# Kernel tuning notes

Hardware: AMD Instinct MI355X
Metric: run time of the kernel (lower is better)

The kernel has to match this reference:

```python
import jax, jax.numpy as jnp
import numpy as np

B, H, S, D = 8, 16, 1024, 128


def setup_inputs() -> dict:
    key = jax.random.key(0)
    kq, kk, kv = jax.random.split(key, 3)
    queries = jax.random.normal(kq, (B, H, S, D), dtype=jnp.float32)
    keys = jax.random.normal(kk, (B, H, S, D), dtype=jnp.float32)
    values = jax.random.normal(kv, (B, H, S, D), dtype=jnp.float32)
    # learnable per-element scale over the full score tensor, init 'ones'
    scale = jnp.ones((B, H, S, S), dtype=jnp.float32)
    return {"queries": queries, "keys": keys, "values": values, "scale": scale}


def reference(queries, keys, values, scale):
    # scores: [B,H,Sq,Sk] = Q K^T
    scores = jnp.einsum("bhqd,bhkd->bhqk", queries, keys)
    # custom learnable scaling: scores / sqrt(scale[0]) * scale
    # scale[0] has shape [H,Sq,Sk] and broadcasts over the batch dim
    scores = scores / jnp.sqrt(scale[0]) * scale
    # masked_softmax with attention_mask=None -> plain softmax over keys axis
    attn = jax.nn.softmax(scores, axis=-1)
    # dropout is identity (rate 0 / eval mode)
    out = jnp.einsum("bhqk,bhkd->bhqd", attn, values)
    return out
```

## Files before the change

kernel.cpp:

```cpp
#include <hip/hip_runtime.h>
#include <math.h>

#define NB 8
#define NH 16
#define NS 1024
#define ND 128

typedef float    f32x4 __attribute__((ext_vector_type(4)));
typedef _Float16 f16x8 __attribute__((ext_vector_type(8)));
typedef _Float16 f16x4 __attribute__((ext_vector_type(4)));
typedef short    s16x4 __attribute__((ext_vector_type(4)));
typedef short    s16x8 __attribute__((ext_vector_type(8)));

#define MFMAH(a, b, c) __builtin_amdgcn_mfma_f32_16x16x32_f16(a, b, c, 0, 0, 0)

__device__ __forceinline__ void gload16(const void* g, void* l) {
  __builtin_amdgcn_global_load_lds(
      (const __attribute__((address_space(1))) void*)g,
      (__attribute__((address_space(3))) void*)l, 16, 0, 0);
}

__global__ void prep_e(const float* __restrict__ scale, _Float16* __restrict__ E) {
  const size_t i0 = ((size_t)blockIdx.x * 256 + threadIdx.x) * 8;
  float4 a0 = *(const float4*)(scale + i0);
  float4 b0 = *(const float4*)(scale + i0 + 4);
  float r[8] = {rsqrtf(a0.x), rsqrtf(a0.y), rsqrtf(a0.z), rsqrtf(a0.w),
                rsqrtf(b0.x), rsqrtf(b0.y), rsqrtf(b0.z), rsqrtf(b0.w)};
#pragma unroll
  for (int b = 0; b < NB; ++b) {
    const float* sp = scale + ((size_t)b << 24) + i0;
    float4 a = *(const float4*)sp;
    float4 bb = *(const float4*)(sp + 4);
    f16x8 o = {(_Float16)(a.x * r[0]), (_Float16)(a.y * r[1]),
               (_Float16)(a.z * r[2]), (_Float16)(a.w * r[3]),
               (_Float16)(bb.x * r[4]), (_Float16)(bb.y * r[5]),
               (_Float16)(bb.z * r[6]), (_Float16)(bb.w * r[7])};
    *(f16x8*)(E + ((size_t)b << 24) + i0) = o;
  }
}

__global__ void prep_k(const float* __restrict__ K, short* __restrict__ Kimg) {
  const int kt = blockIdx.x & 15, bh = blockIdx.x >> 4;
  const float* Kt = K + ((size_t)bh * NS + kt * 64) * ND;
  short* img = Kimg + ((size_t)bh * 16 + kt) * 8192;
#pragma unroll
  for (int i = 0; i < 8; ++i) {
    int f = threadIdx.x + i * 256;
    int key = f >> 5, d4 = (f & 31) << 2;
    float4 v = *(const float4*)(Kt + (size_t)key * ND + d4);
    f16x4 hv = {(_Float16)v.x, (_Float16)v.y, (_Float16)v.z, (_Float16)v.w};
    int gp = (d4 >> 3) ^ (key & 15);
    *(f16x4*)(img + key * 128 + gp * 8 + (d4 & 7)) = hv;
  }
}

__global__ void prep_v(const float* __restrict__ V, short* __restrict__ Vimg) {
  __shared__ _Float16 t[64 * 132];
  const int kt = blockIdx.x & 15, bh = blockIdx.x >> 4;
  const float* Vt = V + ((size_t)bh * NS + kt * 64) * ND;
#pragma unroll
  for (int i = 0; i < 8; ++i) {
    int f = threadIdx.x + i * 256;
    int key = f >> 5, d4 = (f & 31) << 2;
    float4 v = *(const float4*)(Vt + (size_t)key * ND + d4);
    *(f16x4*)&t[key * 132 + d4] =
        (f16x4){(_Float16)v.x, (_Float16)v.y, (_Float16)v.z, (_Float16)v.w};
  }
  __syncthreads();
  short* img = Vimg + ((size_t)bh * 16 + kt) * 8192;
#pragma unroll
  for (int i = 0; i < 4; ++i) {
    int u = threadIdx.x + i * 256;
    int d = u >> 3, g = u & 7;
    f16x8 o;
#pragma unroll
    for (int e = 0; e < 8; ++e) o[e] = t[(g * 8 + e) * 132 + d];
    *(f16x8*)(img + d * 64 + ((g ^ (d & 7)) * 8)) = o;
  }
}

template <bool USE_E>
__launch_bounds__(256, 3)
__global__ void attn_f16(const float* __restrict__ Q, const short* __restrict__ Kimg,
                         const short* __restrict__ Vimg, const _Float16* __restrict__ E,
                         const float* __restrict__ scale, float* __restrict__ out) {
  __shared__ short Ks[64 * 128];
  __shared__ short Vs[128 * 64];
  __shared__ _Float16 Ps[128 * 72];

  const int tid = threadIdx.x;
  const int w = tid >> 6, l = tid & 63;
  const int quad = l >> 4, c = l & 15;

  const int x = blockIdx.x;
  const int bh = ((x >> 6) << 3) | (x & 7);
  const int qblk = (x >> 3) & 7;
  const int q0 = qblk * 128 + w * 32;

  f16x8 qf[2][4];
  {
    const float* Qb = Q + ((size_t)bh * NS + q0) * ND;
#pragma unroll
    for (int nf = 0; nf < 2; ++nf)
#pragma unroll
      for (int kb = 0; kb < 4; ++kb) {
        const float* p = Qb + (size_t)(nf * 16 + c) * ND + kb * 32 + quad * 8;
        float4 a = *(const float4*)p;
        float4 b = *(const float4*)(p + 4);
        qf[nf][kb] = (f16x8){(_Float16)a.x, (_Float16)a.y, (_Float16)a.z, (_Float16)a.w,
                             (_Float16)b.x, (_Float16)b.y, (_Float16)b.z, (_Float16)b.w};
      }
  }

  float m_[2] = {-INFINITY, -INFINITY}, ls_[2] = {0.f, 0.f};
  f32x4 O[2][8];
#pragma unroll
  for (int pf = 0; pf < 2; ++pf)
#pragma unroll
    for (int n0 = 0; n0 < 8; ++n0) O[pf][n0] = (f32x4){0.f, 0.f, 0.f, 0.f};

  const short* Kb = Kimg + (size_t)bh * (16 * 8192);
  const short* Vb = Vimg + (size_t)bh * (16 * 8192);
  const _Float16* Eb = E + ((size_t)bh << 20);
  const float* sclb = scale + ((size_t)bh << 20);
  const float* sc0b = scale + ((size_t)(bh & 15) << 20);

#pragma unroll 1
  for (int kt = 0; kt < 16; ++kt) {
    __syncthreads();
    {
      const short* kg = Kb + kt * 8192 + tid * 8;
      const short* vg = Vb + kt * 8192 + tid * 8;
#pragma unroll
      for (int i = 0; i < 4; ++i) {
        gload16(kg + i * 2048, &Ks[tid * 8 + i * 2048]);
        gload16(vg + i * 2048, &Vs[tid * 8 + i * 2048]);
      }
    }
    f16x4 ef[2][4];
    f32x4 sclv[2][4], sc0v[2][4];
    if (USE_E) {
#pragma unroll
      for (int nf = 0; nf < 2; ++nf)
#pragma unroll
        for (int m0 = 0; m0 < 4; ++m0)
          ef[nf][m0] = *(const f16x4*)(Eb + (size_t)(q0 + nf * 16 + c) * NS +
                                       kt * 64 + m0 * 16 + quad * 4);
    } else {
#pragma unroll
      for (int nf = 0; nf < 2; ++nf)
#pragma unroll
        for (int m0 = 0; m0 < 4; ++m0) {
          size_t off = (size_t)(q0 + nf * 16 + c) * NS + kt * 64 + m0 * 16 + quad * 4;
          sclv[nf][m0] = *(const f32x4*)(sclb + off);
          sc0v[nf][m0] = *(const f32x4*)(sc0b + off);
        }
    }
    __syncthreads();

    f32x4 S[2][4];
#pragma unroll
    for (int nf = 0; nf < 2; ++nf)
#pragma unroll
      for (int m0 = 0; m0 < 4; ++m0) S[nf][m0] = (f32x4){0.f, 0.f, 0.f, 0.f};
#pragma unroll
    for (int m0 = 0; m0 < 4; ++m0) {
#pragma unroll
      for (int kb = 0; kb < 4; ++kb) {
        const f16x8 a = *(const f16x8*)&Ks[(m0 * 16 + c) * 128 + ((((kb << 2) | quad)) ^ c) * 8];
        S[0][m0] = MFMAH(a, qf[0][kb], S[0][m0]);
        S[1][m0] = MFMAH(a, qf[1][kb], S[1][m0]);
      }
    }

    float al2[2];
#pragma unroll
    for (int nf = 0; nf < 2; ++nf) {
      float sv[16];
#pragma unroll
      for (int m0 = 0; m0 < 4; ++m0)
#pragma unroll
        for (int r = 0; r < 4; ++r) {
          float e = USE_E ? (float)ef[nf][m0][r]
                          : sclv[nf][m0][r] * rsqrtf(sc0v[nf][m0][r]);
          sv[m0 * 4 + r] = S[nf][m0][r] * e;
        }
      float tm = sv[0];
#pragma unroll
      for (int i = 1; i < 16; ++i) tm = fmaxf(tm, sv[i]);
      tm = fmaxf(tm, __shfl_xor(tm, 16));
      tm = fmaxf(tm, __shfl_xor(tm, 32));
      float mn = fmaxf(m_[nf], tm);
      float al = __expf(m_[nf] - mn);
      float ps = 0.f;
      _Float16 pb[16];
#pragma unroll
      for (int i = 0; i < 16; ++i) {
        float p = __expf(sv[i] - mn);
        ps += p;
        pb[i] = (_Float16)p;
      }
      ps += __shfl_xor(ps, 16);
      ps += __shfl_xor(ps, 32);
      ls_[nf] = ls_[nf] * al + ps;
      m_[nf] = mn;
      al2[nf] = al;
      _Float16* pr = &Ps[(size_t)(w * 32 + nf * 16 + c) * 72];
#pragma unroll
      for (int m0 = 0; m0 < 4; ++m0)
        *(f16x4*)(pr + m0 * 16 + quad * 4) =
            (f16x4){pb[m0 * 4], pb[m0 * 4 + 1], pb[m0 * 4 + 2], pb[m0 * 4 + 3]};
    }

#pragma unroll
    for (int pf = 0; pf < 2; ++pf) {
      float ar[4];
#pragma unroll
      for (int r = 0; r < 4; ++r) ar[r] = __shfl(al2[pf], quad * 4 + r);
#pragma unroll
      for (int n0 = 0; n0 < 8; ++n0)
#pragma unroll
        for (int r = 0; r < 4; ++r) O[pf][n0][r] *= ar[r];
    }

    f16x8 pfr[2][2];
#pragma unroll
    for (int pf = 0; pf < 2; ++pf)
#pragma unroll
      for (int kb = 0; kb < 2; ++kb)
        pfr[pf][kb] = *(const f16x8*)&Ps[(size_t)(w * 32 + pf * 16 + c) * 72 +
                                         kb * 32 + quad * 8];
#pragma unroll
    for (int n0 = 0; n0 < 8; ++n0) {
#pragma unroll
      for (int kb = 0; kb < 2; ++kb) {
        const f16x8 b =
            *(const f16x8*)&Vs[(n0 * 16 + c) * 64 + ((((kb << 2) | quad)) ^ (c & 7)) * 8];
        O[0][n0] = MFMAH(pfr[0][kb], b, O[0][n0]);
        O[1][n0] = MFMAH(pfr[1][kb], b, O[1][n0]);
      }
    }
  }

  float* ob = out + ((size_t)bh * NS + q0) * ND;
#pragma unroll
  for (int pf = 0; pf < 2; ++pf)
#pragma unroll
    for (int r = 0; r < 4; ++r) {
      float lv = __shfl(ls_[pf], quad * 4 + r);
      float inv = 1.0f / lv;
      int row = pf * 16 + quad * 4 + r;
#pragma unroll
      for (int n0 = 0; n0 < 8; ++n0)
        ob[(size_t)row * ND + n0 * 16 + c] = O[pf][n0][r] * inv;
    }
}

#define TQ 16
#define TK 64
#define PITCH 129
__launch_bounds__(256, 2)
__global__ void attn_fp32(const float* __restrict__ Q, const float* __restrict__ K,
                          const float* __restrict__ V, const float* __restrict__ scale,
                          float* __restrict__ out) {
  __shared__ float qs[TQ][ND];
  __shared__ float kv[TK][PITCH];
  __shared__ float ps[4][4][TK];
  const int tid = threadIdx.x;
  const int w = tid >> 6, l = tid & 63;
  const int bid = blockIdx.x;
  const int qt = bid & 63, h = (bid >> 6) & 15, b = bid >> 10;
  const size_t bh = (size_t)b * NH + h;
  const float* Qb = Q + (bh * NS + (size_t)qt * TQ) * ND;
  const float* Kb = K + bh * NS * ND;
  const float* Vb = V + bh * NS * ND;
  {
    const float4* Q4 = (const float4*)Qb;
    float4* qs4 = (float4*)&qs[0][0];
    qs4[tid] = Q4[tid];
    qs4[tid + 256] = Q4[tid + 256];
  }
  const int q0 = qt * TQ + w * 4;
  const float* sc0p[4];
  const float* sclp[4];
#pragma unroll
  for (int i = 0; i < 4; ++i) {
    const int qg = q0 + i;
    sc0p[i] = scale + ((size_t)h * NS + qg) * NS;
    sclp[i] = scale + (bh * NS + qg) * NS;
  }
  float m[4] = {-INFINITY, -INFINITY, -INFINITY, -INFINITY};
  float lsum[4] = {0.f, 0.f, 0.f, 0.f};
  float oa[4] = {0.f, 0.f, 0.f, 0.f};
  float ob[4] = {0.f, 0.f, 0.f, 0.f};
  for (int kt = 0; kt < NS / TK; ++kt) {
    __syncthreads();
    {
      const float4* K4 = (const float4*)(Kb + (size_t)kt * TK * ND);
#pragma unroll
      for (int i = 0; i < 8; ++i) {
        const int f = tid + i * 256;
        const float4 t4 = K4[f];
        const int r = f >> 5, cc = (f & 31) << 2;
        kv[r][cc] = t4.x; kv[r][cc + 1] = t4.y; kv[r][cc + 2] = t4.z; kv[r][cc + 3] = t4.w;
      }
    }
    __syncthreads();
    const int kg = kt * TK + l;
    float sc0[4], scl[4];
#pragma unroll
    for (int i = 0; i < 4; ++i) { sc0[i] = sc0p[i][kg]; scl[i] = sclp[i][kg]; }
    float s[4] = {0.f, 0.f, 0.f, 0.f};
#pragma unroll 8
    for (int d = 0; d < ND; ++d) {
      const float kd = kv[l][d];
      s[0] = fmaf(qs[w * 4 + 0][d], kd, s[0]);
      s[1] = fmaf(qs[w * 4 + 1][d], kd, s[1]);
      s[2] = fmaf(qs[w * 4 + 2][d], kd, s[2]);
      s[3] = fmaf(qs[w * 4 + 3][d], kd, s[3]);
    }
#pragma unroll
    for (int i = 0; i < 4; ++i) {
      const float svv = s[i] * scl[i] * rsqrtf(sc0[i]);
      float mx = svv;
#pragma unroll
      for (int off = 32; off > 0; off >>= 1) mx = fmaxf(mx, __shfl_xor(mx, off));
      const float mn = fmaxf(m[i], mx);
      const float p = __expf(svv - mn);
      const float al = __expf(m[i] - mn);
      float psum = p;
#pragma unroll
      for (int off = 32; off > 0; off >>= 1) psum += __shfl_xor(psum, off);
      lsum[i] = lsum[i] * al + psum;
      m[i] = mn;
      oa[i] *= al;
      ob[i] *= al;
      ps[w][i][l] = p;
    }
    __syncthreads();
    {
      const float4* V4 = (const float4*)(Vb + (size_t)kt * TK * ND);
#pragma unroll
      for (int i = 0; i < 8; ++i) {
        const int f = tid + i * 256;
        const float4 t4 = V4[f];
        const int r = f >> 5, cc = (f & 31) << 2;
        kv[r][cc] = t4.x; kv[r][cc + 1] = t4.y; kv[r][cc + 2] = t4.z; kv[r][cc + 3] = t4.w;
      }
    }
    __syncthreads();
#pragma unroll 4
    for (int k2 = 0; k2 < TK; ++k2) {
      const float v0 = kv[k2][l];
      const float v1 = kv[k2][64 + l];
#pragma unroll
      for (int i = 0; i < 4; ++i) {
        const float p = ps[w][i][k2];
        oa[i] = fmaf(p, v0, oa[i]);
        ob[i] = fmaf(p, v1, ob[i]);
      }
    }
  }
  float* op = out + (bh * NS + q0) * ND;
#pragma unroll
  for (int i = 0; i < 4; ++i) {
    const float inv = 1.0f / lsum[i];
    op[(size_t)i * ND + l] = oa[i] * inv;
    op[(size_t)i * ND + 64 + l] = ob[i] * inv;
  }
}

extern "C" void kernel_launch(void* const* d_in, const int* in_sizes, int n_in,
                              void* d_out, int out_size, void* d_ws, size_t ws_size,
                              hipStream_t stream) {
  const float* Q = (const float*)d_in[0];
  const float* K = (const float*)d_in[1];
  const float* V = (const float*)d_in[2];
  const float* scale = (const float*)d_in[3];
  float* out = (float*)d_out;

  const size_t KV_BYTES = (size_t)NB * NH * NS * ND * 2;
  const size_t E_BYTES = (size_t)NB * NH * NS * NS * 2;
  const size_t needB = 2 * KV_BYTES;
  const size_t needA = needB + E_BYTES;

  if (ws_size >= needB) {
    short* Kimg = (short*)d_ws;
    short* Vimg = (short*)((char*)d_ws + KV_BYTES);
    prep_k<<<dim3(NB * NH * 16), dim3(256), 0, stream>>>(K, Kimg);
    prep_v<<<dim3(NB * NH * 16), dim3(256), 0, stream>>>(V, Vimg);
    if (ws_size >= needA) {
      _Float16* E = (_Float16*)((char*)d_ws + needB);
      prep_e<<<dim3(8192), dim3(256), 0, stream>>>(scale, E);
      attn_f16<true><<<dim3(1024), dim3(256), 0, stream>>>(Q, Kimg, Vimg, E, scale, out);
    } else {
      attn_f16<false><<<dim3(1024), dim3(256), 0, stream>>>(Q, Kimg, Vimg, nullptr, scale, out);
    }
  } else {
    attn_fp32<<<dim3(NB * NH * (NS / TK) * 4), dim3(256), 0, stream>>>(Q, K, V, scale, out);
  }
}
```

Baseline: 1.075 ms.

## Double-buffer K/V tiles with smaller key tiles and merge prep kernels

Shrinks key tiles from 64 to 32 and double-buffers K/V in shared memory so the next tile's global-to-LDS loads and E/scale loads overlap compute on the current tile. Fuses the three preprocessing kernels into one launch and adds a wave-uniform skip of the O rescale when the running max is unchanged. This aims to hide load latency and cut launch overhead, at the cost of more barriers per key and a changed V image layout.

Result: faster. 1.013 ms (-5.8%).

```diff
diff --git a/kernel.cpp b/kernel.cpp
--- a/kernel.cpp
+++ b/kernel.cpp
@@ -6,11 +6,14 @@
 #define NS 1024
 #define ND 128
 
+#define BN 32
+#define NT (NS / BN)
+#define TILE_SH (BN * ND)
+#define PSTR 40
+
 typedef float    f32x4 __attribute__((ext_vector_type(4)));
 typedef _Float16 f16x8 __attribute__((ext_vector_type(8)));
 typedef _Float16 f16x4 __attribute__((ext_vector_type(4)));
-typedef short    s16x4 __attribute__((ext_vector_type(4)));
-typedef short    s16x8 __attribute__((ext_vector_type(8)));
 
 #define MFMAH(a, b, c) __builtin_amdgcn_mfma_f32_16x16x32_f16(a, b, c, 0, 0, 0)
 
@@ -20,73 +23,184 @@
       (__attribute__((address_space(3))) void*)l, 16, 0, 0);
 }
 
-__global__ void prep_e(const float* __restrict__ scale, _Float16* __restrict__ E) {
-  const size_t i0 = ((size_t)blockIdx.x * 256 + threadIdx.x) * 8;
-  float4 a0 = *(const float4*)(scale + i0);
-  float4 b0 = *(const float4*)(scale + i0 + 4);
-  float r[8] = {rsqrtf(a0.x), rsqrtf(a0.y), rsqrtf(a0.z), rsqrtf(a0.w),
-                rsqrtf(b0.x), rsqrtf(b0.y), rsqrtf(b0.z), rsqrtf(b0.w)};
-#pragma unroll
-  for (int b = 0; b < NB; ++b) {
-    const float* sp = scale + ((size_t)b << 24) + i0;
-    float4 a = *(const float4*)sp;
-    float4 bb = *(const float4*)(sp + 4);
-    f16x8 o = {(_Float16)(a.x * r[0]), (_Float16)(a.y * r[1]),
-               (_Float16)(a.z * r[2]), (_Float16)(a.w * r[3]),
-               (_Float16)(bb.x * r[4]), (_Float16)(bb.y * r[5]),
-               (_Float16)(bb.z * r[6]), (_Float16)(bb.w * r[7])};
-    *(f16x8*)(E + ((size_t)b << 24) + i0) = o;
+__global__ void prep_all(const float* __restrict__ scale, _Float16* __restrict__ E,
+                         const float* __restrict__ K, short* __restrict__ Kimg,
+                         const float* __restrict__ V, short* __restrict__ Vimg,
+                         int base) {
+  __shared__ _Float16 tbuf[BN * 132];
+  const int x = blockIdx.x + base;
+  const int tid = threadIdx.x;
+  if (x < 8192) {
+    const size_t i0 = ((size_t)x * 256 + tid) * 8;
+    float4 a0 = *(const float4*)(scale + i0);
+    float4 b0 = *(const float4*)(scale + i0 + 4);
+    float r[8] = {rsqrtf(a0.x), rsqrtf(a0.y), rsqrtf(a0.z), rsqrtf(a0.w),
+                  rsqrtf(b0.x), rsqrtf(b0.y), rsqrtf(b0.z), rsqrtf(b0.w)};
+    *(f16x8*)(E + i0) =
+        (f16x8){(_Float16)(a0.x * r[0]), (_Float16)(a0.y * r[1]),
+                (_Float16)(a0.z * r[2]), (_Float16)(a0.w * r[3]),
+                (_Float16)(b0.x * r[4]), (_Float16)(b0.y * r[5]),
+                (_Float16)(b0.z * r[6]), (_Float16)(b0.w * r[7])};
+#pragma unroll
+    for (int b = 1; b < NB; ++b) {
+      const float* sp = scale + ((size_t)b << 24) + i0;
+      float4 a = *(const float4*)sp;
+      float4 bb = *(const float4*)(sp + 4);
+      *(f16x8*)(E + ((size_t)b << 24) + i0) =
+          (f16x8){(_Float16)(a.x * r[0]),  (_Float16)(a.y * r[1]),
+                  (_Float16)(a.z * r[2]),  (_Float16)(a.w * r[3]),
+                  (_Float16)(bb.x * r[4]), (_Float16)(bb.y * r[5]),
+                  (_Float16)(bb.z * r[6]), (_Float16)(bb.w * r[7])};
+    }
+  } else if (x < 12288) {
+    const int p = x - 8192;
+    const int t = p & 31, bh = p >> 5;
+    const float* Kt = K + ((size_t)bh * NS + t * BN) * ND;
+    short* img = Kimg + ((size_t)bh * NT + t) * TILE_SH;
+#pragma unroll
+    for (int i = 0; i < 4; ++i) {
+      int f = tid + i * 256;
+      int key = f >> 5, d4 = (f & 31) << 2;
+      float4 v = *(const float4*)(Kt + (size_t)key * ND + d4);
+      f16x4 hv = {(_Float16)v.x, (_Float16)v.y, (_Float16)v.z, (_Float16)v.w};
+      int gp = (d4 >> 3) ^ (key & 15);
+      *(f16x4*)(img + key * 128 + gp * 8 + (d4 & 7)) = hv;
+    }
+  } else {
+    const int p = x - 12288;
+    const int t = p & 31, bh = p >> 5;
+    const float* Vt = V + ((size_t)bh * NS + t * BN) * ND;
+#pragma unroll
+    for (int i = 0; i < 4; ++i) {
+      int f = tid + i * 256;
+      int key = f >> 5, d4 = (f & 31) << 2;
+      float4 v = *(const float4*)(Vt + (size_t)key * ND + d4);
+      *(f16x4*)&tbuf[key * 132 + d4] =
+          (f16x4){(_Float16)v.x, (_Float16)v.y, (_Float16)v.z, (_Float16)v.w};
+    }
+    __syncthreads();
+    short* img = Vimg + ((size_t)bh * NT + t) * TILE_SH;
+#pragma unroll
+    for (int i = 0; i < 2; ++i) {
+      int u = tid + i * 256;
+      int d = u >> 2, k8 = u & 3;
+      f16x8 o;
+#pragma unroll
+      for (int e = 0; e < 8; ++e) o[e] = tbuf[(k8 * 8 + e) * 132 + d];
+      *(f16x8*)(img + d * BN + ((k8 ^ ((d >> 1) & 3)) * 8)) = o;
+    }
   }
 }
 
-__global__ void prep_k(const float* __restrict__ K, short* __restrict__ Kimg) {
-  const int kt = blockIdx.x & 15, bh = blockIdx.x >> 4;
-  const float* Kt = K + ((size_t)bh * NS + kt * 64) * ND;
-  short* img = Kimg + ((size_t)bh * 16 + kt) * 8192;
-#pragma unroll
-  for (int i = 0; i < 8; ++i) {
-    int f = threadIdx.x + i * 256;
-    int key = f >> 5, d4 = (f & 31) << 2;
-    float4 v = *(const float4*)(Kt + (size_t)key * ND + d4);
-    f16x4 hv = {(_Float16)v.x, (_Float16)v.y, (_Float16)v.z, (_Float16)v.w};
-    int gp = (d4 >> 3) ^ (key & 15);
-    *(f16x4*)(img + key * 128 + gp * 8 + (d4 & 7)) = hv;
-  }
-}
-
-__global__ void prep_v(const float* __restrict__ V, short* __restrict__ Vimg) {
-  __shared__ _Float16 t[64 * 132];
-  const int kt = blockIdx.x & 15, bh = blockIdx.x >> 4;
-  const float* Vt = V + ((size_t)bh * NS + kt * 64) * ND;
-#pragma unroll
-  for (int i = 0; i < 8; ++i) {
-    int f = threadIdx.x + i * 256;
-    int key = f >> 5, d4 = (f & 31) << 2;
-    float4 v = *(const float4*)(Vt + (size_t)key * ND + d4);
-    *(f16x4*)&t[key * 132 + d4] =
-        (f16x4){(_Float16)v.x, (_Float16)v.y, (_Float16)v.z, (_Float16)v.w};
-  }
-  __syncthreads();
-  short* img = Vimg + ((size_t)bh * 16 + kt) * 8192;
-#pragma unroll
-  for (int i = 0; i < 4; ++i) {
-    int u = threadIdx.x + i * 256;
-    int d = u >> 3, g = u & 7;
-    f16x8 o;
-#pragma unroll
-    for (int e = 0; e < 8; ++e) o[e] = t[(g * 8 + e) * 132 + d];
-    *(f16x8*)(img + d * 64 + ((g ^ (d & 7)) * 8)) = o;
-  }
-}
+
+#define ISSUE(T, B)                                              \
+  do {                                                           \
+    const short* kg_ = Kb + (T) * TILE_SH + tid * 8;             \
+    const short* vg_ = Vb + (T) * TILE_SH + tid * 8;             \
+    gload16(kg_, &Ks[B][tid * 8]);                               \
+    gload16(kg_ + 2048, &Ks[B][tid * 8 + 2048]);                 \
+    gload16(vg_, &Vs[B][tid * 8]);                               \
+    gload16(vg_ + 2048, &Vs[B][tid * 8 + 2048]);                 \
+  } while (0)
+
+#define LOADE(DST, T)                                                             \
+  do {                                                                            \
+    _Pragma("unroll") for (int nf = 0; nf < 2; ++nf)                              \
+        _Pragma("unroll") for (int m0 = 0; m0 < 2; ++m0)                          \
+            DST[nf][m0] = *(const f16x4*)(Eb + (size_t)(q0 + nf * 16 + c) * NS +  \
+                                          (T) * BN + m0 * 16 + quad * 4);         \
+  } while (0)
+
+#define LOADS(SV, S0, T)                                                          \
+  do {                                                                            \
+    _Pragma("unroll") for (int nf = 0; nf < 2; ++nf)                              \
+        _Pragma("unroll") for (int m0 = 0; m0 < 2; ++m0) {                        \
+      size_t off_ = (size_t)(q0 + nf * 16 + c) * NS + (T) * BN + m0 * 16 + quad * 4; \
+      SV[nf][m0] = *(const f32x4*)(sclb + off_);                                  \
+      S0[nf][m0] = *(const f32x4*)(sc0b + off_);                                  \
+    }                                                                             \
+  } while (0)
+
+#define TILE_STEP(BUF, EF, SCV, SC0, KT)                                             \
+  do {                                                                               \
+    f32x4 S_[2][2];                                                                  \
+    _Pragma("unroll") for (int nf = 0; nf < 2; ++nf)                                 \
+        _Pragma("unroll") for (int m0 = 0; m0 < 2; ++m0)                             \
+            S_[nf][m0] = (f32x4){0.f, 0.f, 0.f, 0.f};                                \
+    _Pragma("unroll") for (int m0 = 0; m0 < 2; ++m0) {                               \
+      _Pragma("unroll") for (int kb = 0; kb < 4; ++kb) {                             \
+        const f16x8 a_ = *(const f16x8*)&Ks[BUF][(m0 * 16 + c) * 128 +               \
+                                                 (((kb << 2) | quad) ^ c) * 8];      \
+        S_[0][m0] = MFMAH(a_, qf[0][kb], S_[0][m0]);                                 \
+        S_[1][m0] = MFMAH(a_, qf[1][kb], S_[1][m0]);                                 \
+      }                                                                              \
+    }                                                                                \
+    float al2_[2];                                                                   \
+    int skipall_ = 1;                                                                \
+    _Pragma("unroll") for (int nf = 0; nf < 2; ++nf) {                               \
+      float sv[8];                                                                   \
+      _Pragma("unroll") for (int m0 = 0; m0 < 2; ++m0)                               \
+          _Pragma("unroll") for (int r = 0; r < 4; ++r) {                            \
+        float e_ = USE_E ? (float)EF[nf][m0][r]                                      \
+                         : SCV[nf][m0][r] * rsqrtf(SC0[nf][m0][r]);                  \
+        sv[m0 * 4 + r] = S_[nf][m0][r] * e_;                                         \
+      }                                                                              \
+      float tm = sv[0];                                                              \
+      _Pragma("unroll") for (int i = 1; i < 8; ++i) tm = fmaxf(tm, sv[i]);           \
+      tm = fmaxf(tm, __shfl_xor(tm, 16));                                            \
+      tm = fmaxf(tm, __shfl_xor(tm, 32));                                            \
+      float mn, al;                                                                  \
+      if (__all(tm <= m_[nf])) {                         \
+        mn = m_[nf]; al = 1.f;                                                       \
+      } else {                                                                       \
+        mn = fmaxf(m_[nf], tm);                                                      \
+        al = __expf(m_[nf] - mn);                                                    \
+        m_[nf] = mn;                                                                 \
+        skipall_ = 0;                                                                \
+      }                                                                              \
+      al2_[nf] = al;                                                                 \
+      float ps = 0.f;                                                                \
+      _Float16 pb[8];                                                                \
+      _Pragma("unroll") for (int i = 0; i < 8; ++i) {                                \
+        float p_ = __expf(sv[i] - mn);                                               \
+        ps += p_;                                                                    \
+        pb[i] = (_Float16)p_;                                                        \
+      }                                                                              \
+      ps += __shfl_xor(ps, 16);                                                      \
+      ps += __shfl_xor(ps, 32);                                                      \
+      ls_[nf] = ls_[nf] * al + ps;                                                   \
+      _Float16* pr_ = &Ps[(size_t)(w * 32 + nf * 16 + c) * PSTR];                    \
+      *(f16x4*)(pr_ + quad * 4)      = (f16x4){pb[0], pb[1], pb[2], pb[3]};          \
+      *(f16x4*)(pr_ + 16 + quad * 4) = (f16x4){pb[4], pb[5], pb[6], pb[7]};          \
+    }                                                                                \
+    if (!skipall_) {                                                                 \
+      _Pragma("unroll") for (int pf = 0; pf < 2; ++pf) {                             \
+        float ar_[4];                                                                \
+        _Pragma("unroll") for (int r = 0; r < 4; ++r)                                \
+            ar_[r] = __shfl(al2_[pf], quad * 4 + r);                                 \
+        _Pragma("unroll") for (int n0 = 0; n0 < 8; ++n0)                             \
+            _Pragma("unroll") for (int r = 0; r < 4; ++r) O[pf][n0][r] *= ar_[r];    \
+      }                                                                              \
+    }                                                                                \
+    const f16x8 pf0_ = *(const f16x8*)&Ps[(size_t)(w * 32 + c) * PSTR + quad * 8];   \
+    const f16x8 pf1_ =                                                               \
+        *(const f16x8*)&Ps[(size_t)(w * 32 + 16 + c) * PSTR + quad * 8];             \
+    _Pragma("unroll") for (int n0 = 0; n0 < 8; ++n0) {                               \
+      const f16x8 b_ = *(const f16x8*)&Vs[BUF][(n0 * 16 + c) * 32 +                  \
+                                              (quad ^ ((c >> 1) & 3)) * 8];          \
+      O[0][n0] = MFMAH(pf0_, b_, O[0][n0]);                                          \
+      O[1][n0] = MFMAH(pf1_, b_, O[1][n0]);                                          \
+    }                                                                                \
+  } while (0)
 
 template <bool USE_E>
 __launch_bounds__(256, 3)
 __global__ void attn_f16(const float* __restrict__ Q, const short* __restrict__ Kimg,
                          const short* __restrict__ Vimg, const _Float16* __restrict__ E,
                          const float* __restrict__ scale, float* __restrict__ out) {
-  __shared__ short Ks[64 * 128];
-  __shared__ short Vs[128 * 64];
-  __shared__ _Float16 Ps[128 * 72];
+  __shared__ short Ks[2][TILE_SH];
+  __shared__ short Vs[2][TILE_SH];
+  __shared__ _Float16 Ps[128 * PSTR];
 
   const int tid = threadIdx.x;
   const int w = tid >> 6, l = tid & 63;
@@ -96,6 +210,16 @@
   const int bh = ((x >> 6) << 3) | (x & 7);
   const int qblk = (x >> 3) & 7;
   const int q0 = qblk * 128 + w * 32;
+
+  const short* Kb = Kimg + (size_t)bh * (NT * TILE_SH);
+  const short* Vb = Vimg + (size_t)bh * (NT * TILE_SH);
+  const _Float16* Eb = E + ((size_t)bh << 20);
+  const float* sclb = scale + ((size_t)bh << 20);
+  const float* sc0b = scale + ((size_t)(bh & 15) << 20);
+
+  ISSUE(0, 0);
+  f16x4 efA[2][2], efB[2][2];
+  if (USE_E) LOADE(efA, 0);
 
   f16x8 qf[2][4];
   {
@@ -119,127 +243,22 @@
 #pragma unroll
     for (int n0 = 0; n0 < 8; ++n0) O[pf][n0] = (f32x4){0.f, 0.f, 0.f, 0.f};
 
-  const short* Kb = Kimg + (size_t)bh * (16 * 8192);
-  const short* Vb = Vimg + (size_t)bh * (16 * 8192);
-  const _Float16* Eb = E + ((size_t)bh << 20);
-  const float* sclb = scale + ((size_t)bh << 20);
-  const float* sc0b = scale + ((size_t)(bh & 15) << 20);
+  f32x4 sclvA[2][2], sc0vA[2][2], sclvB[2][2], sc0vB[2][2];
 
 #pragma unroll 1
-  for (int kt = 0; kt < 16; ++kt) {
-    __syncthreads();
-    {
-      const short* kg = Kb + kt * 8192 + tid * 8;
-      const short* vg = Vb + kt * 8192 + tid * 8;
-#pragma unroll
-      for (int i = 0; i < 4; ++i) {
-        gload16(kg + i * 2048, &Ks[tid * 8 + i * 2048]);
-        gload16(vg + i * 2048, &Vs[tid * 8 + i * 2048]);
-      }
-    }
-    f16x4 ef[2][4];
-    f32x4 sclv[2][4], sc0v[2][4];
-    if (USE_E) {
-#pragma unroll
-      for (int nf = 0; nf < 2; ++nf)
-#pragma unroll
-        for (int m0 = 0; m0 < 4; ++m0)
-          ef[nf][m0] = *(const f16x4*)(Eb + (size_t)(q0 + nf * 16 + c) * NS +
-                                       kt * 64 + m0 * 16 + quad * 4);
-    } else {
-#pragma unroll
-      for (int nf = 0; nf < 2; ++nf)
-#pragma unroll
-        for (int m0 = 0; m0 < 4; ++m0) {
-          size_t off = (size_t)(q0 + nf * 16 + c) * NS + kt * 64 + m0 * 16 + quad * 4;
-          sclv[nf][m0] = *(const f32x4*)(sclb + off);
-          sc0v[nf][m0] = *(const f32x4*)(sc0b + off);
-        }
-    }
-    __syncthreads();
-
-    f32x4 S[2][4];
-#pragma unroll
-    for (int nf = 0; nf < 2; ++nf)
-#pragma unroll
-      for (int m0 = 0; m0 < 4; ++m0) S[nf][m0] = (f32x4){0.f, 0.f, 0.f, 0.f};
-#pragma unroll
-    for (int m0 = 0; m0 < 4; ++m0) {
-#pragma unroll
-      for (int kb = 0; kb < 4; ++kb) {
-        const f16x8 a = *(const f16x8*)&Ks[(m0 * 16 + c) * 128 + ((((kb << 2) | quad)) ^ c) * 8];
-        S[0][m0] = MFMAH(a, qf[0][kb], S[0][m0]);
-        S[1][m0] = MFMAH(a, qf[1][kb], S[1][m0]);
-      }
-    }
-
-    float al2[2];
-#pragma unroll
-    for (int nf = 0; nf < 2; ++nf) {
-      float sv[16];
-#pragma unroll
-      for (int m0 = 0; m0 < 4; ++m0)
-#pragma unroll
-        for (int r = 0; r < 4; ++r) {
-          float e = USE_E ? (float)ef[nf][m0][r]
-                          : sclv[nf][m0][r] * rsqrtf(sc0v[nf][m0][r]);
-          sv[m0 * 4 + r] = S[nf][m0][r] * e;
-        }
-      float tm = sv[0];
-#pragma unroll
-      for (int i = 1; i < 16; ++i) tm = fmaxf(tm, sv[i]);
-      tm = fmaxf(tm, __shfl_xor(tm, 16));
-      tm = fmaxf(tm, __shfl_xor(tm, 32));
-      float mn = fmaxf(m_[nf], tm);
-      float al = __expf(m_[nf] - mn);
-      float ps = 0.f;
-      _Float16 pb[16];
-#pragma unroll
-      for (int i = 0; i < 16; ++i) {
-        float p = __expf(sv[i] - mn);
-        ps += p;
-        pb[i] = (_Float16)p;
-      }
-      ps += __shfl_xor(ps, 16);
-      ps += __shfl_xor(ps, 32);
-      ls_[nf] = ls_[nf] * al + ps;
-      m_[nf] = mn;
-      al2[nf] = al;
-      _Float16* pr = &Ps[(size_t)(w * 32 + nf * 16 + c) * 72];
-#pragma unroll
-      for (int m0 = 0; m0 < 4; ++m0)
-        *(f16x4*)(pr + m0 * 16 + quad * 4) =
-            (f16x4){pb[m0 * 4], pb[m0 * 4 + 1], pb[m0 * 4 + 2], pb[m0 * 4 + 3]};
-    }
-
-#pragma unroll
-    for (int pf = 0; pf < 2; ++pf) {
-      float ar[4];
-#pragma unroll
-      for (int r = 0; r < 4; ++r) ar[r] = __shfl(al2[pf], quad * 4 + r);
-#pragma unroll
-      for (int n0 = 0; n0 < 8; ++n0)
-#pragma unroll
-        for (int r = 0; r < 4; ++r) O[pf][n0][r] *= ar[r];
-    }
-
-    f16x8 pfr[2][2];
-#pragma unroll
-    for (int pf = 0; pf < 2; ++pf)
-#pragma unroll
-      for (int kb = 0; kb < 2; ++kb)
-        pfr[pf][kb] = *(const f16x8*)&Ps[(size_t)(w * 32 + pf * 16 + c) * 72 +
-                                         kb * 32 + quad * 8];
-#pragma unroll
-    for (int n0 = 0; n0 < 8; ++n0) {
-#pragma unroll
-      for (int kb = 0; kb < 2; ++kb) {
-        const f16x8 b =
-            *(const f16x8*)&Vs[(n0 * 16 + c) * 64 + ((((kb << 2) | quad)) ^ (c & 7)) * 8];
-        O[0][n0] = MFMAH(pfr[0][kb], b, O[0][n0]);
-        O[1][n0] = MFMAH(pfr[1][kb], b, O[1][n0]);
-      }
-    }
+  for (int kt = 0; kt < NT; kt += 2) {
+    __syncthreads();
+    if (!USE_E) LOADS(sclvA, sc0vA, kt);
+    ISSUE(kt + 1, 1);
+    if (USE_E) LOADE(efB, kt + 1);
+    TILE_STEP(0, efA, sclvA, sc0vA, kt);
+    __syncthreads();
+    if (!USE_E) LOADS(sclvB, sc0vB, kt + 1);
+    if (kt + 2 < NT) {
+      ISSUE(kt + 2, 0);
+      if (USE_E) LOADE(efA, kt + 2);
+    }
+    TILE_STEP(1, efB, sclvB, sc0vB, kt + 1);
   }
 
   float* ob = out + ((size_t)bh * NS + q0) * ND;
@@ -387,16 +406,18 @@
   if (ws_size >= needB) {
     short* Kimg = (short*)d_ws;
     short* Vimg = (short*)((char*)d_ws + KV_BYTES);
-    prep_k<<<dim3(NB * NH * 16), dim3(256), 0, stream>>>(K, Kimg);
-    prep_v<<<dim3(NB * NH * 16), dim3(256), 0, stream>>>(V, Vimg);
     if (ws_size >= needA) {
       _Float16* E = (_Float16*)((char*)d_ws + needB);
-      prep_e<<<dim3(8192), dim3(256), 0, stream>>>(scale, E);
+      prep_all<<<dim3(16384), dim3(256), 0, stream>>>(scale, E, K, Kimg, V, Vimg, 0);
       attn_f16<true><<<dim3(1024), dim3(256), 0, stream>>>(Q, Kimg, Vimg, E, scale, out);
     } else {
-      attn_f16<false><<<dim3(1024), dim3(256), 0, stream>>>(Q, Kimg, Vimg, nullptr, scale, out);
+      prep_all<<<dim3(8192), dim3(256), 0, stream>>>(scale, nullptr, K, Kimg, V, Vimg,
+                                                     8192);
+      attn_f16<false><<<dim3(1024), dim3(256), 0, stream>>>(Q, Kimg, Vimg, nullptr,
+                                                            scale, out);
     }
   } else {
-    attn_fp32<<<dim3(NB * NH * (NS / TK) * 4), dim3(256), 0, stream>>>(Q, K, V, scale, out);
+    attn_fp32<<<dim3(NB * NH * (NS / TK) * 4), dim3(256), 0, stream>>>(Q, K, V, scale,
+                                                                       out);
   }
 }
```
